# Optimization experiments

Measured on AMD Instinct MI355X. Metric: run time of the kernel, lower is better.

Reference implementation:

```python
import jax, jax.numpy as jnp
import numpy as np

VOCAB = 32000
EMB = 512       # embedding_size; also the sequence length per the source loop
HID = 512       # hidden_dim
NTAG = 36       # number of POS-tag-specific LSTMCells
OUT = 1         # output_size
SEQ = EMB       # forward iterates range(embedding_size)


def setup_inputs() -> dict:
    key = jax.random.key(0)
    ks = jax.random.split(key, 10)
    s = 1.0 / np.sqrt(HID)  # torch LSTMCell init: U(-1/sqrt(H), 1/sqrt(H))
    inp = {
        "x": jax.random.randint(ks[0], (1, SEQ), 0, VOCAB, dtype=jnp.int64)
             if jax.config.jax_enable_x64 else
             jax.random.randint(ks[0], (1, SEQ), 0, VOCAB, dtype=jnp.int32),
        "tag_ids": jax.random.randint(ks[1], (SEQ,), 0, NTAG, dtype=jnp.int32),
        "h0": jnp.zeros((1, HID), jnp.float32),
        "c0": jnp.zeros((1, HID), jnp.float32),
        # frozen pretrained embedding table
        "emb": jax.random.normal(ks[2], (VOCAB, EMB), jnp.float32) * 0.1,
        # stacked per-tag LSTMCell params, torch gate order (i, f, g, o)
        "W_ih": jax.random.uniform(ks[3], (NTAG, 4 * HID, EMB), jnp.float32, -s, s),
        "W_hh": jax.random.uniform(ks[4], (NTAG, 4 * HID, HID), jnp.float32, -s, s),
        "b_ih": jax.random.uniform(ks[5], (NTAG, 4 * HID), jnp.float32, -s, s),
        "b_hh": jax.random.uniform(ks[6], (NTAG, 4 * HID), jnp.float32, -s, s),
        "W_fc": jax.random.uniform(ks[7], (OUT, HID), jnp.float32, -s, s),
        "b_fc": jax.random.uniform(ks[8], (OUT,), jnp.float32, -s, s),
    }
    return inp


def _lstm_cell(x_t, h, c, Wih, Whh, bih, bhh):
    # x_t: [D], h/c: [H]; Wih: [4H, D], Whh: [4H, H]
    gates = Wih @ x_t + Whh @ h + bih + bhh      # [4H]
    i, f, g, o = jnp.split(gates, 4)
    i, f, o = jax.nn.sigmoid(i), jax.nn.sigmoid(f), jax.nn.sigmoid(o)
    g = jnp.tanh(g)
    c_new = f * c + i * g
    h_new = o * jnp.tanh(c_new)
    return h_new, c_new


def reference(x, tag_ids, h0, c0, emb, W_ih, W_hh, b_ih, b_hh, W_fc, b_fc):
    embeds = emb[x[0]]                            # [T, D] (batch is structurally 1)

    def step(carry, xs):
        h, c = carry
        x_t, tag = xs
        h, c = _lstm_cell(x_t, h, c, W_ih[tag], W_hh[tag], b_ih[tag], b_hh[tag])
        return (h, c), None

    (h, c), _ = jax.lax.scan(step, (h0[0], c0[0]), (embeds, tag_ids))
    # dropout is identity in eval; fc + sigmoid; out[:, -1]
    out = jax.nn.sigmoid(h @ W_fc.T + b_fc)       # [OUT]
    out = out.reshape(1, -1)[:, -1]               # [1]
    return out, h[None, :], c[None, :]
```

## Files before the change

### kernel.cpp

```cpp
#include <hip/hip_runtime.h>

#define VOCAB 32000
#define EMB 512
#define HID 512
#define NTAG 36
#define SEQ 512
#define G4H 2048
#define NBLK 128
#define XCHUNK 32

typedef unsigned long long ull;

__device__ __forceinline__ float fast_tanh(float x) {
    float e = __expf(2.f * x);
    return 1.f - 2.f / (e + 1.f);
}
__device__ __forceinline__ float fast_sigmoid(float x) {
    return 1.f / (1.f + __expf(-x));
}

__global__ __launch_bounds__(256) void precompute_z(
    const int* __restrict__ x,
    const int* __restrict__ tag_ids,
    const float* __restrict__ emb,
    const float* __restrict__ W_ih,
    const float* __restrict__ b_ih,
    const float* __restrict__ b_hh,
    float* __restrict__ Z)
{
    __shared__ int list[SEQ];
    __shared__ int cnt;
    __shared__ __align__(16) float xc[XCHUNK][EMB];

    const int tid  = threadIdx.x;
    const int tag  = blockIdx.x;
    const int row0 = blockIdx.y * 64;
    const int wave = tid >> 6, lane = tid & 63;

    if (tid == 0) cnt = 0;
    __syncthreads();
    for (int t = tid; t < SEQ; t += 256)
        if (tag_ids[t] == tag) { int p = atomicAdd(&cnt, 1); list[p] = t; }
    __syncthreads();
    const int n = cnt;

    for (int c0 = 0; c0 < n; c0 += XCHUNK) {
        const int nc = min(XCHUNK, n - c0);
        __syncthreads();
        for (int idx = tid; idx < nc * 128; idx += 256) {
            int tl = idx >> 7, k4 = idx & 127;
            int t = list[c0 + tl];
            ((float4*)xc[tl])[k4] = ((const float4*)(emb + (size_t)x[t] * EMB))[k4];
        }
        __syncthreads();
        for (int rr = 0; rr < 16; rr += 4) {
            const int row = row0 + wave * 16 + rr;
            const float* w0p = W_ih + ((size_t)tag * G4H + row) * EMB;
            const float* w1p = w0p + EMB;
            const float* w2p = w0p + 2 * EMB;
            const float* w3p = w0p + 3 * EMB;
            const float4 wa0 = ((const float4*)w0p)[lane], wa1 = ((const float4*)w0p)[64 + lane];
            const float4 wb0 = ((const float4*)w1p)[lane], wb1 = ((const float4*)w1p)[64 + lane];
            const float4 wc0 = ((const float4*)w2p)[lane], wc1 = ((const float4*)w2p)[64 + lane];
            const float4 wd0 = ((const float4*)w3p)[lane], wd1 = ((const float4*)w3p)[64 + lane];
            const float bi0 = b_ih[tag * G4H + row]     + b_hh[tag * G4H + row];
            const float bi1 = b_ih[tag * G4H + row + 1] + b_hh[tag * G4H + row + 1];
            const float bi2 = b_ih[tag * G4H + row + 2] + b_hh[tag * G4H + row + 2];
            const float bi3 = b_ih[tag * G4H + row + 3] + b_hh[tag * G4H + row + 3];
            for (int tl = 0; tl < nc; ++tl) {
                float4 x0 = *(const float4*)&xc[tl][4 * lane];
                float4 x1 = *(const float4*)&xc[tl][256 + 4 * lane];
                float d0 = wa0.x*x0.x + wa0.y*x0.y + wa0.z*x0.z + wa0.w*x0.w
                         + wa1.x*x1.x + wa1.y*x1.y + wa1.z*x1.z + wa1.w*x1.w;
                float d1 = wb0.x*x0.x + wb0.y*x0.y + wb0.z*x0.z + wb0.w*x0.w
                         + wb1.x*x1.x + wb1.y*x1.y + wb1.z*x1.z + wb1.w*x1.w;
                float d2 = wc0.x*x0.x + wc0.y*x0.y + wc0.z*x0.z + wc0.w*x0.w
                         + wc1.x*x1.x + wc1.y*x1.y + wc1.z*x1.z + wc1.w*x1.w;
                float d3 = wd0.x*x0.x + wd0.y*x0.y + wd0.z*x0.z + wd0.w*x0.w
                         + wd1.x*x1.x + wd1.y*x1.y + wd1.z*x1.z + wd1.w*x1.w;
                #pragma unroll
                for (int m = 32; m >= 1; m >>= 1) {
                    d0 += __shfl_xor(d0, m, 64);
                    d1 += __shfl_xor(d1, m, 64);
                    d2 += __shfl_xor(d2, m, 64);
                    d3 += __shfl_xor(d3, m, 64);
                }
                if (lane == 0) {
                    float* zr = Z + (size_t)list[c0 + tl] * G4H + row;
                    zr[0] = d0 + bi0; zr[1] = d1 + bi1;
                    zr[2] = d2 + bi2; zr[3] = d3 + bi3;
                }
            }
        }
    }
}

__global__ __launch_bounds__(256) void lstm_seq(
    const int* __restrict__ tag_ids,
    const float* __restrict__ h0,
    const float* __restrict__ c0,
    const float* __restrict__ W_hh,
    const float* __restrict__ Z,
    const float* __restrict__ W_fc,
    const float* __restrict__ b_fc,
    ull* __restrict__ hist,
    float* __restrict__ d_out)
{
    __shared__ int tags[SEQ];
    __shared__ __align__(16) float hsh[2][HID];
    __shared__ float red[256];

    const int tid  = threadIdx.x;
    const int b    = blockIdx.x;
    const int wave = tid >> 6, lane = tid & 63;
    const int j    = b * 4 + wave;

    for (int t = tid; t < SEQ; t += 256) tags[t] = tag_ids[t];
    __syncthreads();

    float c    = (lane == 0) ? c0[j] : 0.f;
    float hval = 0.f;

    for (int t = 0; t < SEQ; ++t) {
        const int tag = tags[t];
        const float* wbase = W_hh + (size_t)tag * G4H * HID;
        const float4* r;
        r = (const float4*)(wbase + (size_t)(j)        * HID);
        float4 wi0 = r[lane], wi1 = r[64 + lane];
        r = (const float4*)(wbase + (size_t)(512 + j)  * HID);
        float4 wf0 = r[lane], wf1 = r[64 + lane];
        r = (const float4*)(wbase + (size_t)(1024 + j) * HID);
        float4 wg0 = r[lane], wg1 = r[64 + lane];
        r = (const float4*)(wbase + (size_t)(1536 + j) * HID);
        float4 wo0 = r[lane], wo1 = r[64 + lane];

        float zi = 0.f, zf = 0.f, zg = 0.f, zo = 0.f;
        if (lane == 0) {
            const float* zt = Z + (size_t)t * G4H;
            zi = zt[j]; zf = zt[512 + j]; zg = zt[1024 + j]; zo = zt[1536 + j];
        }

        asm volatile("s_waitcnt vmcnt(0)" ::: "memory");

        float v0, v1;
        if (t == 0) {
            v0 = h0[2 * tid]; v1 = h0[2 * tid + 1];
        } else {
            const ull* pa = hist + (size_t)(t - 1) * HID + 2 * tid;
            const ull* pb = pa + 1;
            const unsigned want = (unsigned)t;
            ull a0 = __hip_atomic_load(pa, __ATOMIC_RELAXED, __HIP_MEMORY_SCOPE_AGENT);
            ull b0 = __hip_atomic_load(pb, __ATOMIC_RELAXED, __HIP_MEMORY_SCOPE_AGENT);
            ull a1 = __hip_atomic_load(pa, __ATOMIC_RELAXED, __HIP_MEMORY_SCOPE_AGENT);
            ull b1 = __hip_atomic_load(pb, __ATOMIC_RELAXED, __HIP_MEMORY_SCOPE_AGENT);
            ull a2 = __hip_atomic_load(pa, __ATOMIC_RELAXED, __HIP_MEMORY_SCOPE_AGENT);
            ull b2 = __hip_atomic_load(pb, __ATOMIC_RELAXED, __HIP_MEMORY_SCOPE_AGENT);
            while ((unsigned)(a0 >> 32) != want || (unsigned)(b0 >> 32) != want) {
                a0 = a1; b0 = b1;
                a1 = a2; b1 = b2;
                a2 = __hip_atomic_load(pa, __ATOMIC_RELAXED, __HIP_MEMORY_SCOPE_AGENT);
                b2 = __hip_atomic_load(pb, __ATOMIC_RELAXED, __HIP_MEMORY_SCOPE_AGENT);
            }
            v0 = __uint_as_float((unsigned)a0);
            v1 = __uint_as_float((unsigned)b0);
        }
        const int hb = t & 1;
        hsh[hb][2 * tid]     = v0;
        hsh[hb][2 * tid + 1] = v1;
        __syncthreads();

        const float4 ha = *(const float4*)&hsh[hb][4 * lane];
        const float4 hc = *(const float4*)&hsh[hb][256 + 4 * lane];

        float di = wi0.x*ha.x + wi0.y*ha.y + wi0.z*ha.z + wi0.w*ha.w
                 + wi1.x*hc.x + wi1.y*hc.y + wi1.z*hc.z + wi1.w*hc.w;
        float df = wf0.x*ha.x + wf0.y*ha.y + wf0.z*ha.z + wf0.w*ha.w
                 + wf1.x*hc.x + wf1.y*hc.y + wf1.z*hc.z + wf1.w*hc.w;
        float dg = wg0.x*ha.x + wg0.y*ha.y + wg0.z*ha.z + wg0.w*ha.w
                 + wg1.x*hc.x + wg1.y*hc.y + wg1.z*hc.z + wg1.w*hc.w;
        float do_ = wo0.x*ha.x + wo0.y*ha.y + wo0.z*ha.z + wo0.w*ha.w
                  + wo1.x*hc.x + wo1.y*hc.y + wo1.z*hc.z + wo1.w*hc.w;
        #pragma unroll
        for (int m = 32; m >= 1; m >>= 1) {
            di  += __shfl_xor(di,  m, 64);
            df  += __shfl_xor(df,  m, 64);
            dg  += __shfl_xor(dg,  m, 64);
            do_ += __shfl_xor(do_, m, 64);
        }

        if (lane == 0) {
            float gi = zi + di, gf = zf + df, gg = zg + dg, go = zo + do_;
            float si = fast_sigmoid(gi);
            float sf = fast_sigmoid(gf);
            float so = fast_sigmoid(go);
            float tg = fast_tanh(gg);
            c = sf * c + si * tg;
            hval = so * fast_tanh(c);
            ull pk = ((ull)(unsigned)(t + 1) << 32) | (ull)__float_as_uint(hval);
            __hip_atomic_store(&hist[(size_t)t * HID + j], pk,
                               __ATOMIC_RELAXED, __HIP_MEMORY_SCOPE_AGENT);
        }
    }

    if (lane == 0) {
        d_out[1 + j]       = hval;
        d_out[1 + HID + j] = c;
    }

    if (b == 0) {
        const ull* hp = hist + (size_t)(SEQ - 1) * HID;
        ull a  = __hip_atomic_load(&hp[2 * tid],     __ATOMIC_RELAXED, __HIP_MEMORY_SCOPE_AGENT);
        ull bq = __hip_atomic_load(&hp[2 * tid + 1], __ATOMIC_RELAXED, __HIP_MEMORY_SCOPE_AGENT);
        while ((unsigned)(a >> 32) != (unsigned)SEQ || (unsigned)(bq >> 32) != (unsigned)SEQ) {
            a  = __hip_atomic_load(&hp[2 * tid],     __ATOMIC_RELAXED, __HIP_MEMORY_SCOPE_AGENT);
            bq = __hip_atomic_load(&hp[2 * tid + 1], __ATOMIC_RELAXED, __HIP_MEMORY_SCOPE_AGENT);
        }
        float s = __uint_as_float((unsigned)a)  * W_fc[2 * tid]
                + __uint_as_float((unsigned)bq) * W_fc[2 * tid + 1];
        red[tid] = s;
        __syncthreads();
        #pragma unroll
        for (int off = 128; off > 0; off >>= 1) {
            if (tid < off) red[tid] += red[tid + off];
            __syncthreads();
        }
        if (tid == 0)
            d_out[0] = fast_sigmoid(red[0] + b_fc[0]);
    }
}

extern "C" void kernel_launch(void* const* d_in, const int* in_sizes, int n_in,
                              void* d_out, int out_size, void* d_ws, size_t ws_size,
                              hipStream_t stream) {
    const int*   x       = (const int*)d_in[0];
    const int*   tag_ids = (const int*)d_in[1];
    const float* h0      = (const float*)d_in[2];
    const float* c0      = (const float*)d_in[3];
    const float* emb     = (const float*)d_in[4];
    const float* W_ih    = (const float*)d_in[5];
    const float* W_hh    = (const float*)d_in[6];
    const float* b_ih    = (const float*)d_in[7];
    const float* b_hh    = (const float*)d_in[8];
    const float* W_fc    = (const float*)d_in[9];
    const float* b_fc    = (const float*)d_in[10];
    float* out = (float*)d_out;

    const size_t zBytes = (size_t)SEQ * G4H * sizeof(float);
    float* Z    = (float*)d_ws;
    ull*   hist = (ull*)((char*)d_ws + zBytes);

    dim3 gA(NTAG, 32);
    precompute_z<<<gA, 256, 0, stream>>>(x, tag_ids, emb, W_ih, b_ih, b_hh, Z);
    lstm_seq<<<NBLK, 256, 0, stream>>>(tag_ids, h0, c0, W_hh, Z, W_fc, b_fc,
                                       hist, out);
}
```

Before: 1.331 ms.

## Prefetch next step's W_hh rows and Z into double-buffered registers

Restructures the recurrent loop to issue the global loads of the next timestep's per-tag W_hh rows and precomputed Z values while the current step is spinning on and consuming the hidden state. Two register sets alternate via an unrolled-by-two loop, and the blanket vmcnt(0) wait is replaced by an lgkmcnt wait plus raw barrier. This is meant to hide weight-fetch latency behind the cross-block synchronization on the serial critical path. It doubles weight register usage and relies on the compiler inserting correct vmcnt waits before the prefetched registers are used.

```diff
diff --git a/kernel.cpp b/kernel.cpp
--- a/kernel.cpp
+++ b/kernel.cpp
@@ -121,86 +121,115 @@
     float c    = (lane == 0) ? c0[j] : 0.f;
     float hval = 0.f;
 
-    for (int t = 0; t < SEQ; ++t) {
-        const int tag = tags[t];
-        const float* wbase = W_hh + (size_t)tag * G4H * HID;
-        const float4* r;
-        r = (const float4*)(wbase + (size_t)(j)        * HID);
-        float4 wi0 = r[lane], wi1 = r[64 + lane];
-        r = (const float4*)(wbase + (size_t)(512 + j)  * HID);
-        float4 wf0 = r[lane], wf1 = r[64 + lane];
-        r = (const float4*)(wbase + (size_t)(1024 + j) * HID);
-        float4 wg0 = r[lane], wg1 = r[64 + lane];
-        r = (const float4*)(wbase + (size_t)(1536 + j) * HID);
-        float4 wo0 = r[lane], wo1 = r[64 + lane];
-
-        float zi = 0.f, zf = 0.f, zg = 0.f, zo = 0.f;
-        if (lane == 0) {
-            const float* zt = Z + (size_t)t * G4H;
-            zi = zt[j]; zf = zt[512 + j]; zg = zt[1024 + j]; zo = zt[1536 + j];
-        }
-
-        asm volatile("s_waitcnt vmcnt(0)" ::: "memory");
-
-        float v0, v1;
-        if (t == 0) {
-            v0 = h0[2 * tid]; v1 = h0[2 * tid + 1];
-        } else {
-            const ull* pa = hist + (size_t)(t - 1) * HID + 2 * tid;
-            const ull* pb = pa + 1;
-            const unsigned want = (unsigned)t;
-            ull a0 = __hip_atomic_load(pa, __ATOMIC_RELAXED, __HIP_MEMORY_SCOPE_AGENT);
-            ull b0 = __hip_atomic_load(pb, __ATOMIC_RELAXED, __HIP_MEMORY_SCOPE_AGENT);
-            ull a1 = __hip_atomic_load(pa, __ATOMIC_RELAXED, __HIP_MEMORY_SCOPE_AGENT);
-            ull b1 = __hip_atomic_load(pb, __ATOMIC_RELAXED, __HIP_MEMORY_SCOPE_AGENT);
-            ull a2 = __hip_atomic_load(pa, __ATOMIC_RELAXED, __HIP_MEMORY_SCOPE_AGENT);
-            ull b2 = __hip_atomic_load(pb, __ATOMIC_RELAXED, __HIP_MEMORY_SCOPE_AGENT);
-            while ((unsigned)(a0 >> 32) != want || (unsigned)(b0 >> 32) != want) {
-                a0 = a1; b0 = b1;
-                a1 = a2; b1 = b2;
-                a2 = __hip_atomic_load(pa, __ATOMIC_RELAXED, __HIP_MEMORY_SCOPE_AGENT);
-                b2 = __hip_atomic_load(pb, __ATOMIC_RELAXED, __HIP_MEMORY_SCOPE_AGENT);
-            }
-            v0 = __uint_as_float((unsigned)a0);
-            v1 = __uint_as_float((unsigned)b0);
-        }
-        const int hb = t & 1;
-        hsh[hb][2 * tid]     = v0;
-        hsh[hb][2 * tid + 1] = v1;
-        __syncthreads();
-
-        const float4 ha = *(const float4*)&hsh[hb][4 * lane];
-        const float4 hc = *(const float4*)&hsh[hb][256 + 4 * lane];
-
-        float di = wi0.x*ha.x + wi0.y*ha.y + wi0.z*ha.z + wi0.w*ha.w
-                 + wi1.x*hc.x + wi1.y*hc.y + wi1.z*hc.z + wi1.w*hc.w;
-        float df = wf0.x*ha.x + wf0.y*ha.y + wf0.z*ha.z + wf0.w*ha.w
-                 + wf1.x*hc.x + wf1.y*hc.y + wf1.z*hc.z + wf1.w*hc.w;
-        float dg = wg0.x*ha.x + wg0.y*ha.y + wg0.z*ha.z + wg0.w*ha.w
-                 + wg1.x*hc.x + wg1.y*hc.y + wg1.z*hc.z + wg1.w*hc.w;
-        float do_ = wo0.x*ha.x + wo0.y*ha.y + wo0.z*ha.z + wo0.w*ha.w
-                  + wo1.x*hc.x + wo1.y*hc.y + wo1.z*hc.z + wo1.w*hc.w;
-        #pragma unroll
-        for (int m = 32; m >= 1; m >>= 1) {
-            di  += __shfl_xor(di,  m, 64);
-            df  += __shfl_xor(df,  m, 64);
-            dg  += __shfl_xor(dg,  m, 64);
-            do_ += __shfl_xor(do_, m, 64);
-        }
-
-        if (lane == 0) {
-            float gi = zi + di, gf = zf + df, gg = zg + dg, go = zo + do_;
-            float si = fast_sigmoid(gi);
-            float sf = fast_sigmoid(gf);
-            float so = fast_sigmoid(go);
-            float tg = fast_tanh(gg);
-            c = sf * c + si * tg;
-            hval = so * fast_tanh(c);
-            ull pk = ((ull)(unsigned)(t + 1) << 32) | (ull)__float_as_uint(hval);
-            __hip_atomic_store(&hist[(size_t)t * HID + j], pk,
-                               __ATOMIC_RELAXED, __HIP_MEMORY_SCOPE_AGENT);
-        }
-    }
+    float4 A0, A1, A2, A3, A4, A5, A6, A7;
+    float4 B0, B1, B2, B3, B4, B5, B6, B7;
+    float  Azi = 0.f, Azf = 0.f, Azg = 0.f, Azo = 0.f;
+    float  Bzi = 0.f, Bzf = 0.f, Bzg = 0.f, Bzo = 0.f;
+
+#define ISSUE(T, W0,W1,W2,W3,W4,W5,W6,W7, ZI,ZF,ZG,ZO)                       \
+    do {                                                                      \
+        const int tg_ = tags[(T)];                                            \
+        const float* wb_ = W_hh + (size_t)tg_ * (size_t)G4H * HID;            \
+        const float4* r_;                                                     \
+        r_ = (const float4*)(wb_ + (size_t)(j)        * HID);                 \
+        W0 = r_[lane];  W1 = r_[64 + lane];                                   \
+        r_ = (const float4*)(wb_ + (size_t)(512 + j)  * HID);                 \
+        W2 = r_[lane];  W3 = r_[64 + lane];                                   \
+        r_ = (const float4*)(wb_ + (size_t)(1024 + j) * HID);                 \
+        W4 = r_[lane];  W5 = r_[64 + lane];                                   \
+        r_ = (const float4*)(wb_ + (size_t)(1536 + j) * HID);                 \
+        W6 = r_[lane];  W7 = r_[64 + lane];                                   \
+        if (lane == 0) {                                                      \
+            const float* zt_ = Z + (size_t)(T) * G4H;                         \
+            ZI = zt_[j];        ZF = zt_[512 + j];                            \
+            ZG = zt_[1024 + j]; ZO = zt_[1536 + j];                           \
+        }                                                                     \
+        asm volatile("" ::: "memory");                                        \
+    } while (0)
+
+#define STEP(T, W0,W1,W2,W3,W4,W5,W6,W7, ZI,ZF,ZG,ZO,                         \
+                N0,N1,N2,N3,N4,N5,N6,N7, NZI,NZF,NZG,NZO)                     \
+    do {                                                                      \
+        const int t_ = (T);                                                   \
+        float v0_, v1_;                                                       \
+        if (t_ == 0) {                                                        \
+            v0_ = h0[2 * tid]; v1_ = h0[2 * tid + 1];                         \
+        } else {                                                              \
+            const ull* pa_ = hist + (size_t)(t_ - 1) * HID + 2 * tid;         \
+            const ull* pb_ = pa_ + 1;                                         \
+            const unsigned want_ = (unsigned)t_;                              \
+             \
+              \
+            ull a0_ = __hip_atomic_load(pa_, __ATOMIC_RELAXED, __HIP_MEMORY_SCOPE_AGENT); \
+            ull b0_ = __hip_atomic_load(pb_, __ATOMIC_RELAXED, __HIP_MEMORY_SCOPE_AGENT); \
+            ull a1_ = __hip_atomic_load(pa_, __ATOMIC_RELAXED, __HIP_MEMORY_SCOPE_AGENT); \
+            ull b1_ = __hip_atomic_load(pb_, __ATOMIC_RELAXED, __HIP_MEMORY_SCOPE_AGENT); \
+            ull a2_ = __hip_atomic_load(pa_, __ATOMIC_RELAXED, __HIP_MEMORY_SCOPE_AGENT); \
+            ull b2_ = __hip_atomic_load(pb_, __ATOMIC_RELAXED, __HIP_MEMORY_SCOPE_AGENT); \
+            while ((unsigned)(a0_ >> 32) != want_ ||                          \
+                   (unsigned)(b0_ >> 32) != want_) {                          \
+                a0_ = a1_; b0_ = b1_;                                         \
+                a1_ = a2_; b1_ = b2_;                                         \
+                a2_ = __hip_atomic_load(pa_, __ATOMIC_RELAXED, __HIP_MEMORY_SCOPE_AGENT); \
+                b2_ = __hip_atomic_load(pb_, __ATOMIC_RELAXED, __HIP_MEMORY_SCOPE_AGENT); \
+            }                                                                 \
+            v0_ = __uint_as_float((unsigned)a0_);                             \
+            v1_ = __uint_as_float((unsigned)b0_);                             \
+        }                                                                     \
+         \
+         \
+        if (t_ + 1 < SEQ)                                                     \
+            ISSUE(t_ + 1, N0,N1,N2,N3,N4,N5,N6,N7, NZI,NZF,NZG,NZO);          \
+        const int hb_ = t_ & 1;                                               \
+        hsh[hb_][2 * tid]     = v0_;                                          \
+        hsh[hb_][2 * tid + 1] = v1_;                                          \
+        \
+        asm volatile("s_waitcnt lgkmcnt(0)" ::: "memory");                    \
+        __builtin_amdgcn_s_barrier();                                         \
+        __builtin_amdgcn_sched_barrier(0);                                    \
+        const float4 ha_ = *(const float4*)&hsh[hb_][4 * lane];               \
+        const float4 hc_ = *(const float4*)&hsh[hb_][256 + 4 * lane];         \
+        float di_  = W0.x*ha_.x + W0.y*ha_.y + W0.z*ha_.z + W0.w*ha_.w        \
+                   + W1.x*hc_.x + W1.y*hc_.y + W1.z*hc_.z + W1.w*hc_.w;       \
+        float df_  = W2.x*ha_.x + W2.y*ha_.y + W2.z*ha_.z + W2.w*ha_.w        \
+                   + W3.x*hc_.x + W3.y*hc_.y + W3.z*hc_.z + W3.w*hc_.w;       \
+        float dg_  = W4.x*ha_.x + W4.y*ha_.y + W4.z*ha_.z + W4.w*ha_.w        \
+                   + W5.x*hc_.x + W5.y*hc_.y + W5.z*hc_.z + W5.w*hc_.w;       \
+        float do2_ = W6.x*ha_.x + W6.y*ha_.y + W6.z*ha_.z + W6.w*ha_.w        \
+                   + W7.x*hc_.x + W7.y*hc_.y + W7.z*hc_.z + W7.w*hc_.w;       \
+        _Pragma("unroll")                                                     \
+        for (int m_ = 32; m_ >= 1; m_ >>= 1) {                                \
+            di_  += __shfl_xor(di_,  m_, 64);                                 \
+            df_  += __shfl_xor(df_,  m_, 64);                                 \
+            dg_  += __shfl_xor(dg_,  m_, 64);                                 \
+            do2_ += __shfl_xor(do2_, m_, 64);                                 \
+        }                                                                     \
+        if (lane == 0) {                                                      \
+            float gi_ = ZI + di_,  gf_ = ZF + df_;                            \
+            float gg_ = ZG + dg_,  go_ = ZO + do2_;                           \
+            float si_  = fast_sigmoid(gi_);                                   \
+            float sf_  = fast_sigmoid(gf_);                                   \
+            float so_  = fast_sigmoid(go_);                                   \
+            float tg2_ = fast_tanh(gg_);                                      \
+            c = sf_ * c + si_ * tg2_;                                         \
+            hval = so_ * fast_tanh(c);                                        \
+            ull pk_ = ((ull)(unsigned)(t_ + 1) << 32)                         \
+                    | (ull)__float_as_uint(hval);                             \
+            __hip_atomic_store(&hist[(size_t)t_ * HID + j], pk_,              \
+                               __ATOMIC_RELAXED, __HIP_MEMORY_SCOPE_AGENT);   \
+        }                                                                     \
+    } while (0)
+
+    ISSUE(0, A0,A1,A2,A3,A4,A5,A6,A7, Azi,Azf,Azg,Azo);
+
+    for (int t = 0; t < SEQ; t += 2) {
+        STEP(t,     A0,A1,A2,A3,A4,A5,A6,A7, Azi,Azf,Azg,Azo,
+                    B0,B1,B2,B3,B4,B5,B6,B7, Bzi,Bzf,Bzg,Bzo);
+        STEP(t + 1, B0,B1,B2,B3,B4,B5,B6,B7, Bzi,Bzf,Bzg,Bzo,
+                    A0,A1,A2,A3,A4,A5,A6,A7, Azi,Azf,Azg,Azo);
+    }
+#undef STEP
+#undef ISSUE
 
     if (lane == 0) {
         d_out[1 + j]       = hval;
```

Result: slower. 2.831 ms (+112.7%).
